# Optimization experiments

Measured on AMD Instinct MI355X. Metric: run time of the kernel, lower is better.

The kernel has to match this reference:

```python
import jax, jax.numpy as jnp
import numpy as np

D_MODEL = 512
NUM_HEADS = 8
DEPTH = D_MODEL // NUM_HEADS
B, S = 8, 1024


def setup_inputs() -> dict:
    key = jax.random.key(0)
    ks = jax.random.split(key, 14)
    scale = 1.0 / np.sqrt(D_MODEL)
    inp = {
        "q_in": jax.random.normal(ks[0], (B, S, D_MODEL), jnp.float32),
        "k_in": jax.random.normal(ks[1], (B, S, D_MODEL), jnp.float32),
        "v_in": jax.random.normal(ks[2], (B, S, D_MODEL), jnp.float32),
        # padding mask: 1 = masked-out position
        "mask": jax.random.randint(ks[3], (B, 1, 1, S), 0, 2).astype(jnp.float32),
        "additional_weights": jax.random.uniform(ks[4], (B, S, S), jnp.float32),
        "wq": jax.random.normal(ks[5], (D_MODEL, D_MODEL), jnp.float32) * scale,
        "bq": jnp.zeros((D_MODEL,), jnp.float32),
        "wk": jax.random.normal(ks[6], (D_MODEL, D_MODEL), jnp.float32) * scale,
        "bk": jnp.zeros((D_MODEL,), jnp.float32),
        "wv": jax.random.normal(ks[7], (D_MODEL, D_MODEL), jnp.float32) * scale,
        "bv": jnp.zeros((D_MODEL,), jnp.float32),
        "wo": jax.random.normal(ks[8], (D_MODEL, D_MODEL), jnp.float32) * scale,
        "bo": jnp.zeros((D_MODEL,), jnp.float32),
    }
    return inp


def _split_heads(x):
    # [B, S, d_model] -> [B, H, S, depth]
    b, s, _ = x.shape
    return x.reshape(b, s, NUM_HEADS, DEPTH).transpose(0, 2, 1, 3)


def reference(q_in, k_in, v_in, mask, additional_weights,
              wq, bq, wk, bk, wv, bv, wo, bo):
    q = _split_heads(q_in @ wq + bq)  # [B,H,S,D]
    k = _split_heads(k_in @ wk + bk)
    v = _split_heads(v_in @ wv + bv)

    scores = jnp.einsum("bhqd,bhkd->bhqk", q, k) / jnp.sqrt(
        jnp.asarray(DEPTH, q.dtype))
    scores = scores + mask * -1e9
    attn = jax.nn.softmax(scores, axis=-1)
    # post-softmax multiplicative weights, broadcast over heads
    attn = attn * additional_weights[:, None, :, :]
    x = jnp.einsum("bhqk,bhkd->bhqd", attn, v)
    x = x.transpose(0, 2, 1, 3).reshape(q_in.shape[0], -1, D_MODEL)
    out = x @ wo + bo
    return out, attn
```

## Files before the change

kernel.cpp:

```cpp
#include <hip/hip_runtime.h>
#include <stdint.h>

typedef unsigned short u16;
typedef short bf16x8 __attribute__((ext_vector_type(8)));
typedef short bf16x4 __attribute__((ext_vector_type(4)));
typedef float f32x4 __attribute__((ext_vector_type(4)));
typedef u16 u16x8 __attribute__((ext_vector_type(8)));
typedef u16 u16x4 __attribute__((ext_vector_type(4)));

#define NHEADS 8
#define SEQ 1024
#define DM 512
#define DEPTH 64
#define BATCH 8
#define BK 32
#define LDSROW 40

__device__ __forceinline__ u16 f2bf(float f) {
    union { float f; unsigned u; } v; v.f = f;
    unsigned r = v.u + 0x7FFF + ((v.u >> 16) & 1);
    return (u16)(r >> 16);
}

__device__ __forceinline__ f32x4 mfma_16x16x16_bf16(bf16x4 a, bf16x4 b, f32x4 c) {
#if __has_builtin(__builtin_amdgcn_mfma_f32_16x16x16bf16_1k)
    return __builtin_amdgcn_mfma_f32_16x16x16bf16_1k(a, b, c, 0, 0, 0);
#else
    asm("v_mfma_f32_16x16x16_bf16 %0, %1, %2, %0" : "+v"(c) : "v"(a), "v"(b));
    return c;
#endif
}

__global__ void __launch_bounds__(256) transpose512(
    const float* __restrict__ w0, const float* __restrict__ w1,
    const float* __restrict__ w2, const float* __restrict__ w3,
    u16* __restrict__ wt)
{
    __shared__ float tile[32][33];
    const float* w = (blockIdx.z == 0) ? w0 : (blockIdx.z == 1) ? w1
                   : (blockIdx.z == 2) ? w2 : w3;
    u16* o = wt + (size_t)blockIdx.z * (DM * DM);
    int rb = blockIdx.y * 32, cb = blockIdx.x * 32;
    int tx = threadIdx.x, ty = threadIdx.y;
    #pragma unroll
    for (int k = 0; k < 32; k += 8)
        tile[ty + k][tx] = w[(size_t)(rb + ty + k) * DM + cb + tx];
    __syncthreads();
    #pragma unroll
    for (int k = 0; k < 32; k += 8)
        o[(size_t)(cb + ty + k) * DM + rb + tx] = f2bf(tile[tx][ty + k]);
}

template <int LAYOUT, int AF32>
__device__ __forceinline__ void gemm_tile2(
    const void* __restrict__ Asrc, const u16* __restrict__ wt,
    const float* __restrict__ bias, void* __restrict__ out_)
{
    __shared__ u16 Al[2][128 * LDSROW];
    __shared__ u16 Bl[2][128 * LDSROW];

    const int tid = threadIdx.x;
    const int wid = tid >> 6, lane = tid & 63;
    const int wm = wid >> 1, wn = wid & 1;
    const int lr = lane & 15, g = lane >> 4, lk = g * 8;
    const int mb = blockIdx.y * 128;
    const int nb = blockIdx.x * 128;
    const int r0 = tid >> 2;
    const int c0 = (tid & 3) * 8;

    f32x4 fa0a, fa0b, fa1a, fa1b;
    u16x8 ua0, ua1, ub0, ub1;

    auto loadStage = [&](int ks) {
        if (AF32) {
            const float* A = (const float*)Asrc;
            fa0a = *(const f32x4*)(A + (size_t)(mb + r0) * DM + ks + c0);
            fa0b = *(const f32x4*)(A + (size_t)(mb + r0) * DM + ks + c0 + 4);
            fa1a = *(const f32x4*)(A + (size_t)(mb + 64 + r0) * DM + ks + c0);
            fa1b = *(const f32x4*)(A + (size_t)(mb + 64 + r0) * DM + ks + c0 + 4);
        } else {
            const u16* A = (const u16*)Asrc;
            ua0 = *(const u16x8*)(A + (size_t)(mb + r0) * DM + ks + c0);
            ua1 = *(const u16x8*)(A + (size_t)(mb + 64 + r0) * DM + ks + c0);
        }
        ub0 = *(const u16x8*)(wt + (size_t)(nb + r0) * DM + ks + c0);
        ub1 = *(const u16x8*)(wt + (size_t)(nb + 64 + r0) * DM + ks + c0);
    };
    auto writeStage = [&](int buf) {
        u16x8 w0, w1;
        if (AF32) {
            #pragma unroll
            for (int j = 0; j < 4; j++) {
                w0[j] = f2bf(fa0a[j]); w0[j + 4] = f2bf(fa0b[j]);
                w1[j] = f2bf(fa1a[j]); w1[j + 4] = f2bf(fa1b[j]);
            }
        } else { w0 = ua0; w1 = ua1; }
        *(u16x8*)(&Al[buf][r0 * LDSROW + c0]) = w0;
        *(u16x8*)(&Al[buf][(64 + r0) * LDSROW + c0]) = w1;
        *(u16x8*)(&Bl[buf][r0 * LDSROW + c0]) = ub0;
        *(u16x8*)(&Bl[buf][(64 + r0) * LDSROW + c0]) = ub1;
    };

    f32x4 acc[4][4];
    #pragma unroll
    for (int i = 0; i < 4; i++)
        #pragma unroll
        for (int j = 0; j < 4; j++) acc[i][j] = (f32x4)0.f;

    loadStage(0);
    for (int ks = 0, step = 0; ks < DM; ks += BK, step++) {
        const int buf = step & 1;
        writeStage(buf);
        if (ks + BK < DM) loadStage(ks + BK);
        __syncthreads();

        bf16x8 af[4], bf4[4];
        #pragma unroll
        for (int mt = 0; mt < 4; mt++)
            af[mt] = *(const bf16x8*)(&Al[buf][(wm * 64 + mt * 16 + lr) * LDSROW + lk]);
        #pragma unroll
        for (int nt = 0; nt < 4; nt++)
            bf4[nt] = *(const bf16x8*)(&Bl[buf][(wn * 64 + nt * 16 + lr) * LDSROW + lk]);
        #pragma unroll
        for (int mt = 0; mt < 4; mt++)
            #pragma unroll
            for (int nt = 0; nt < 4; nt++) {
                if (LAYOUT == 1)
                    acc[mt][nt] = __builtin_amdgcn_mfma_f32_16x16x32_bf16(
                        bf4[nt], af[mt], acc[mt][nt], 0, 0, 0);
                else
                    acc[mt][nt] = __builtin_amdgcn_mfma_f32_16x16x32_bf16(
                        af[mt], bf4[nt], acc[mt][nt], 0, 0, 0);
            }
    }

    #pragma unroll
    for (int mt = 0; mt < 4; mt++) {
        #pragma unroll
        for (int nt = 0; nt < 4; nt++) {
            #pragma unroll
            for (int r = 0; r < 4; r++) {
                if (LAYOUT == 1) {
                    int m = mb + wm * 64 + mt * 16 + lr;
                    int n = nb + wn * 64 + nt * 16 + 4 * g + r;
                    float val = acc[mt][nt][r] + bias[n];
                    int b_ = m >> 10, s = m & 1023, h = n >> 6, d = n & 63;
                    ((u16*)out_)[((size_t)((b_ * NHEADS + h) << 6) + d) * SEQ + s] = f2bf(val);
                } else {
                    int n = nb + wn * 64 + nt * 16 + lr;
                    int m = mb + wm * 64 + mt * 16 + 4 * g + r;
                    float val = acc[mt][nt][r] + bias[n];
                    if (LAYOUT == 2) {
                        ((float*)out_)[(size_t)m * DM + n] = val;
                    } else {
                        int b_ = m >> 10, s = m & 1023, h = n >> 6, d = n & 63;
                        ((u16*)out_)[(((size_t)(b_ * NHEADS + h) * SEQ + s) << 6) + d] = f2bf(val);
                    }
                }
            }
        }
    }
}

__global__ void __launch_bounds__(256) qkv_proj(
    const float* __restrict__ q_in, const float* __restrict__ k_in,
    const float* __restrict__ v_in, const u16* __restrict__ wt_base,
    const float* __restrict__ bq, const float* __restrict__ bk,
    const float* __restrict__ bv,
    u16* __restrict__ Qb, u16* __restrict__ Kb, u16* __restrict__ VTb)
{
    int z = blockIdx.z;
    if (z == 0)      gemm_tile2<0, 1>(q_in, wt_base,              bq, Qb);
    else if (z == 1) gemm_tile2<0, 1>(k_in, wt_base + DM * DM,    bk, Kb);
    else             gemm_tile2<1, 1>(v_in, wt_base + 2 * DM * DM, bv, VTb);
}

__global__ void __launch_bounds__(256) out_proj(
    const u16* __restrict__ X, const u16* __restrict__ wto,
    const float* __restrict__ bo, float* __restrict__ out)
{
    gemm_tile2<2, 0>(X, wto, bo, out);
}

__global__ void __launch_bounds__(256, 5) attn_kernel(
    const u16* __restrict__ Q, const u16* __restrict__ K,
    const u16* __restrict__ VT, const float* __restrict__ mask,
    const float* __restrict__ addw, float* __restrict__ attn_out,
    u16* __restrict__ X)
{
    __shared__ float Xr[4][16][64];
    __shared__ float redm[4][16];
    __shared__ float reds[4][16];

    const int id = blockIdx.x;
    const int c = id & 7, t = id >> 3;
    const int h = t & 7;
    const int p = ((t >> 3) << 3) | c;
    const int qt = p & 63, b = p >> 6;

    const int tid = threadIdx.x, wid = tid >> 6, lane = tid & 63;
    const int lr = lane & 15, g = lane >> 4, lk = g * 8;
    const size_t head = (size_t)(b * NHEADS + h) * (SEQ * DEPTH);
    const u16* Qh = Q + head + (size_t)qt * 16 * DEPTH;
    const u16* Kh = K + head;
    const u16* Vh = VT + head;
    const int wbase = wid << 8;

    bf16x8 qf0 = *(const bf16x8*)(Qh + lr * DEPTH + lk);
    bf16x8 qf1 = *(const bf16x8*)(Qh + lr * DEPTH + 32 + lk);
    f32x4 acc[16];
    #pragma unroll
    for (int nt = 0; nt < 16; nt++) acc[nt] = (f32x4)0.f;
    #pragma unroll
    for (int nt = 0; nt < 16; nt++) {
        const u16* kp = Kh + (size_t)(wbase + (nt << 4) + lr) * DEPTH + lk;
        bf16x8 k0 = *(const bf16x8*)kp;
        bf16x8 k1 = *(const bf16x8*)(kp + 32);
        acc[nt] = __builtin_amdgcn_mfma_f32_16x16x32_bf16(k0, qf0, acc[nt], 0, 0, 0);
        acc[nt] = __builtin_amdgcn_mfma_f32_16x16x32_bf16(k1, qf1, acc[nt], 0, 0, 0);
    }

    const float* mrow = mask + ((size_t)b << 10);
    float mx = -3.0e38f;
    #pragma unroll
    for (int nt = 0; nt < 16; nt++) {
        f32x4 mr = *(const f32x4*)(mrow + wbase + (nt << 4) + 4 * g);
        #pragma unroll
        for (int r = 0; r < 4; r++) {
            acc[nt][r] = acc[nt][r] * 0.125f + mr[r] * -1e9f;
            mx = fmaxf(mx, acc[nt][r]);
        }
    }
    mx = fmaxf(mx, __shfl_xor(mx, 16, 64));
    mx = fmaxf(mx, __shfl_xor(mx, 32, 64));
    if (lane < 16) redm[wid][lr] = mx;
    __syncthreads();
    float gm = fmaxf(fmaxf(redm[0][lr], redm[1][lr]),
                     fmaxf(redm[2][lr], redm[3][lr]));

    float sm = 0.f;
    #pragma unroll
    for (int nt = 0; nt < 16; nt++)
        #pragma unroll
        for (int r = 0; r < 4; r++) {
            float pv = __expf(acc[nt][r] - gm);
            acc[nt][r] = pv;
            sm += pv;
        }
    sm += __shfl_xor(sm, 16, 64);
    sm += __shfl_xor(sm, 32, 64);
    if (lane < 16) reds[wid][lr] = sm;
    __syncthreads();
    float iv = 1.0f / (reds[0][lr] + reds[1][lr] + reds[2][lr] + reds[3][lr]);

    const int qglob = (qt << 4) + lr;
    const size_t awbase = ((size_t)((b << 10) + qglob)) << 10;
    const size_t aobase = ((size_t)(((b * NHEADS + h) << 10) + qglob)) << 10;
    const u16* vb_base = Vh + (size_t)lr * SEQ;

    f32x4 x[4];
    #pragma unroll
    for (int dt = 0; dt < 4; dt++) x[dt] = (f32x4)0.f;

    #pragma unroll
    for (int nt = 0; nt < 16; nt++) {
        const int kk = wbase + (nt << 4) + 4 * g;
        f32x4 aw = *(const f32x4*)(addw + awbase + kk);
        f32x4 o;
        bf16x4 pa;
        #pragma unroll
        for (int r = 0; r < 4; r++) {
            float v = acc[nt][r] * iv * aw[r];
            o[r] = v;
            pa[r] = (short)f2bf(v);
        }
        *(f32x4*)(attn_out + aobase + kk) = o;
        #pragma unroll
        for (int dt = 0; dt < 4; dt++) {
            bf16x4 vb = *(const bf16x4*)(vb_base + (size_t)(dt << 4) * SEQ + kk);
            x[dt] = mfma_16x16x16_bf16(pa, vb, x[dt]);
        }
    }

    #pragma unroll
    for (int dt = 0; dt < 4; dt++)
        #pragma unroll
        for (int r = 0; r < 4; r++)
            Xr[wid][4 * g + r][(dt << 4) + lr] = x[dt][r];
    __syncthreads();

    #pragma unroll
    for (int r = 0; r < 4; r++) {
        int q = 4 * g + r, d = (wid << 4) + lr;
        float s = Xr[0][q][d] + Xr[1][q][d] + Xr[2][q][d] + Xr[3][q][d];
        X[((size_t)((b << 10) + (qt << 4) + q)) * DM + (h << 6) + d] = f2bf(s);
    }
}

extern "C" void kernel_launch(void* const* d_in, const int* in_sizes, int n_in,
                              void* d_out, int out_size, void* d_ws, size_t ws_size,
                              hipStream_t stream)
{
    const float* q_in = (const float*)d_in[0];
    const float* k_in = (const float*)d_in[1];
    const float* v_in = (const float*)d_in[2];
    const float* mask = (const float*)d_in[3];
    const float* addw = (const float*)d_in[4];
    const float* wq = (const float*)d_in[5];
    const float* bq = (const float*)d_in[6];
    const float* wk = (const float*)d_in[7];
    const float* bk = (const float*)d_in[8];
    const float* wv = (const float*)d_in[9];
    const float* bv = (const float*)d_in[10];
    const float* wo = (const float*)d_in[11];
    const float* bo = (const float*)d_in[12];

    const size_t ACT = (size_t)BATCH * SEQ * DM;

    u16* ws = (u16*)d_ws;
    u16* wt  = ws;
    u16* Qb  = wt + 4 * DM * DM;
    u16* Kb  = Qb + ACT;
    u16* VTb = Kb + ACT;
    u16* Xb  = VTb + ACT;

    float* out0 = (float*)d_out;
    float* attn_out = out0 + ACT;

    transpose512<<<dim3(16, 16, 4), dim3(32, 8), 0, stream>>>(wq, wk, wv, wo, wt);
    qkv_proj<<<dim3(4, 64, 3), 256, 0, stream>>>(q_in, k_in, v_in, wt,
                                                 bq, bk, bv, Qb, Kb, VTb);
    attn_kernel<<<dim3(4096), 256, 0, stream>>>(Qb, Kb, VTb, mask, addw,
                                                attn_out, Xb);
    out_proj<<<dim3(4, 64, 1), 256, 0, stream>>>(Xb, wt + 3 * DM * DM, bo, out0);
}
```

Measured before the change: 602.1 us.

## Restructure attention block to 512 threads with LDS-staged P for PV MFMA

The attention kernel now uses 8 waves per 16-query tile, so each wave covers 128 keys. Probabilities are written as bf16 into a padded LDS buffer. The PV product is then redone with 16x16x32 MFMAs, each wave taking one 16-wide depth slice over half the keys, with a 2-way cross-wave reduction. The grid changes to a 3D (head, qtile, batch) order, which drops the old block-id swizzle that grouped heads for addw reuse. Nontemporal loads and stores are added for the streaming addw/attn outputs and the GEMM epilogues. The aim is more parallelism and wider MFMAs, at the cost of extra LDS traffic and a third barrier.

```diff
diff --git a/kernel.cpp b/kernel.cpp
--- a/kernel.cpp
+++ b/kernel.cpp
@@ -15,6 +15,7 @@
 #define BATCH 8
 #define BK 32
 #define LDSROW 40
+#define PSTRIDE 1032
 
 __device__ __forceinline__ u16 f2bf(float f) {
     union { float f; unsigned u; } v; v.f = f;
@@ -22,12 +23,20 @@
     return (u16)(r >> 16);
 }
 
-__device__ __forceinline__ f32x4 mfma_16x16x16_bf16(bf16x4 a, bf16x4 b, f32x4 c) {
-#if __has_builtin(__builtin_amdgcn_mfma_f32_16x16x16bf16_1k)
-    return __builtin_amdgcn_mfma_f32_16x16x16bf16_1k(a, b, c, 0, 0, 0);
+template <typename T>
+__device__ __forceinline__ void st_nt(T* p, T v) {
+#if __has_builtin(__builtin_nontemporal_store)
+    __builtin_nontemporal_store(v, p);
 #else
-    asm("v_mfma_f32_16x16x16_bf16 %0, %1, %2, %0" : "+v"(c) : "v"(a), "v"(b));
-    return c;
+    *p = v;
+#endif
+}
+template <typename T>
+__device__ __forceinline__ T ld_nt(const T* p) {
+#if __has_builtin(__builtin_nontemporal_load)
+    return __builtin_nontemporal_load(p);
+#else
+    return *p;
 #endif
 }
 
@@ -145,16 +154,16 @@
                     int n = nb + wn * 64 + nt * 16 + 4 * g + r;
                     float val = acc[mt][nt][r] + bias[n];
                     int b_ = m >> 10, s = m & 1023, h = n >> 6, d = n & 63;
-                    ((u16*)out_)[((size_t)((b_ * NHEADS + h) << 6) + d) * SEQ + s] = f2bf(val);
+                    st_nt(&((u16*)out_)[((size_t)((b_ * NHEADS + h) << 6) + d) * SEQ + s], f2bf(val));
                 } else {
                     int n = nb + wn * 64 + nt * 16 + lr;
                     int m = mb + wm * 64 + mt * 16 + 4 * g + r;
                     float val = acc[mt][nt][r] + bias[n];
                     if (LAYOUT == 2) {
-                        ((float*)out_)[(size_t)m * DM + n] = val;
+                        st_nt(&((float*)out_)[(size_t)m * DM + n], val);
                     } else {
                         int b_ = m >> 10, s = m & 1023, h = n >> 6, d = n & 63;
-                        ((u16*)out_)[(((size_t)(b_ * NHEADS + h) * SEQ + s) << 6) + d] = f2bf(val);
+                        st_nt(&((u16*)out_)[(((size_t)(b_ * NHEADS + h) * SEQ + s) << 6) + d], f2bf(val));
                     }
                 }
             }
@@ -170,8 +179,8 @@
     u16* __restrict__ Qb, u16* __restrict__ Kb, u16* __restrict__ VTb)
 {
     int z = blockIdx.z;
-    if (z == 0)      gemm_tile2<0, 1>(q_in, wt_base,              bq, Qb);
-    else if (z == 1) gemm_tile2<0, 1>(k_in, wt_base + DM * DM,    bk, Kb);
+    if (z == 0)      gemm_tile2<0, 1>(q_in, wt_base,               bq, Qb);
+    else if (z == 1) gemm_tile2<0, 1>(k_in, wt_base + DM * DM,     bk, Kb);
     else             gemm_tile2<1, 1>(v_in, wt_base + 2 * DM * DM, bv, VTb);
 }
 
@@ -182,37 +191,33 @@
     gemm_tile2<2, 0>(X, wto, bo, out);
 }
 
-__global__ void __launch_bounds__(256, 5) attn_kernel(
+__global__ void __launch_bounds__(512, 6) attn_kernel(
     const u16* __restrict__ Q, const u16* __restrict__ K,
     const u16* __restrict__ VT, const float* __restrict__ mask,
     const float* __restrict__ addw, float* __restrict__ attn_out,
     u16* __restrict__ X)
 {
-    __shared__ float Xr[4][16][64];
-    __shared__ float redm[4][16];
-    __shared__ float reds[4][16];
-
-    const int id = blockIdx.x;
-    const int c = id & 7, t = id >> 3;
-    const int h = t & 7;
-    const int p = ((t >> 3) << 3) | c;
-    const int qt = p & 63, b = p >> 6;
-
+    __shared__ u16 Pl[16 * PSTRIDE];
+    __shared__ float Xr[2][16][64];
+    __shared__ float redm[8][16];
+    __shared__ float reds[8][16];
+
+    const int h = blockIdx.x, qt = blockIdx.y, b = blockIdx.z;
     const int tid = threadIdx.x, wid = tid >> 6, lane = tid & 63;
     const int lr = lane & 15, g = lane >> 4, lk = g * 8;
     const size_t head = (size_t)(b * NHEADS + h) * (SEQ * DEPTH);
     const u16* Qh = Q + head + (size_t)qt * 16 * DEPTH;
     const u16* Kh = K + head;
     const u16* Vh = VT + head;
-    const int wbase = wid << 8;
+    const int wbase = wid << 7;
 
     bf16x8 qf0 = *(const bf16x8*)(Qh + lr * DEPTH + lk);
     bf16x8 qf1 = *(const bf16x8*)(Qh + lr * DEPTH + 32 + lk);
-    f32x4 acc[16];
-    #pragma unroll
-    for (int nt = 0; nt < 16; nt++) acc[nt] = (f32x4)0.f;
-    #pragma unroll
-    for (int nt = 0; nt < 16; nt++) {
+    f32x4 acc[8];
+    #pragma unroll
+    for (int nt = 0; nt < 8; nt++) acc[nt] = (f32x4)0.f;
+    #pragma unroll
+    for (int nt = 0; nt < 8; nt++) {
         const u16* kp = Kh + (size_t)(wbase + (nt << 4) + lr) * DEPTH + lk;
         bf16x8 k0 = *(const bf16x8*)kp;
         bf16x8 k1 = *(const bf16x8*)(kp + 32);
@@ -223,7 +228,7 @@
     const float* mrow = mask + ((size_t)b << 10);
     float mx = -3.0e38f;
     #pragma unroll
-    for (int nt = 0; nt < 16; nt++) {
+    for (int nt = 0; nt < 8; nt++) {
         f32x4 mr = *(const f32x4*)(mrow + wbase + (nt << 4) + 4 * g);
         #pragma unroll
         for (int r = 0; r < 4; r++) {
@@ -235,12 +240,13 @@
     mx = fmaxf(mx, __shfl_xor(mx, 32, 64));
     if (lane < 16) redm[wid][lr] = mx;
     __syncthreads();
-    float gm = fmaxf(fmaxf(redm[0][lr], redm[1][lr]),
-                     fmaxf(redm[2][lr], redm[3][lr]));
+    float gm = redm[0][lr];
+    #pragma unroll
+    for (int w = 1; w < 8; w++) gm = fmaxf(gm, redm[w][lr]);
 
     float sm = 0.f;
     #pragma unroll
-    for (int nt = 0; nt < 16; nt++)
+    for (int nt = 0; nt < 8; nt++)
         #pragma unroll
         for (int r = 0; r < 4; r++) {
             float pv = __expf(acc[nt][r] - gm);
@@ -251,49 +257,51 @@
     sm += __shfl_xor(sm, 32, 64);
     if (lane < 16) reds[wid][lr] = sm;
     __syncthreads();
-    float iv = 1.0f / (reds[0][lr] + reds[1][lr] + reds[2][lr] + reds[3][lr]);
+    float sv = reds[0][lr];
+    #pragma unroll
+    for (int w = 1; w < 8; w++) sv += reds[w][lr];
+    float iv = 1.0f / sv;
 
     const int qglob = (qt << 4) + lr;
     const size_t awbase = ((size_t)((b << 10) + qglob)) << 10;
     const size_t aobase = ((size_t)(((b * NHEADS + h) << 10) + qglob)) << 10;
-    const u16* vb_base = Vh + (size_t)lr * SEQ;
-
-    f32x4 x[4];
-    #pragma unroll
-    for (int dt = 0; dt < 4; dt++) x[dt] = (f32x4)0.f;
-
-    #pragma unroll
-    for (int nt = 0; nt < 16; nt++) {
+    #pragma unroll
+    for (int nt = 0; nt < 8; nt++) {
         const int kk = wbase + (nt << 4) + 4 * g;
-        f32x4 aw = *(const f32x4*)(addw + awbase + kk);
+        f32x4 aw = ld_nt((const f32x4*)(addw + awbase + kk));
         f32x4 o;
-        bf16x4 pa;
+        u16x4 pb;
         #pragma unroll
         for (int r = 0; r < 4; r++) {
             float v = acc[nt][r] * iv * aw[r];
             o[r] = v;
-            pa[r] = (short)f2bf(v);
-        }
-        *(f32x4*)(attn_out + aobase + kk) = o;
-        #pragma unroll
-        for (int dt = 0; dt < 4; dt++) {
-            bf16x4 vb = *(const bf16x4*)(vb_base + (size_t)(dt << 4) * SEQ + kk);
-            x[dt] = mfma_16x16x16_bf16(pa, vb, x[dt]);
-        }
-    }
-
-    #pragma unroll
-    for (int dt = 0; dt < 4; dt++)
-        #pragma unroll
-        for (int r = 0; r < 4; r++)
-            Xr[wid][4 * g + r][(dt << 4) + lr] = x[dt][r];
-    __syncthreads();
-
-    #pragma unroll
-    for (int r = 0; r < 4; r++) {
-        int q = 4 * g + r, d = (wid << 4) + lr;
-        float s = Xr[0][q][d] + Xr[1][q][d] + Xr[2][q][d] + Xr[3][q][d];
-        X[((size_t)((b << 10) + (qt << 4) + q)) * DM + (h << 6) + d] = f2bf(s);
+            pb[r] = f2bf(v);
+        }
+        st_nt((f32x4*)(attn_out + aobase + kk), o);
+        *(u16x4*)(Pl + lr * PSTRIDE + kk) = pb;
+    }
+    __syncthreads();
+
+    const int kh = wid >> 2, dq = wid & 3;
+    f32x4 x = (f32x4)0.f;
+    const u16* vrow = Vh + (size_t)((dq << 4) + lr) * SEQ;
+    const int ks0 = kh << 9;
+    for (int ks = ks0; ks < ks0 + 512; ks += 32) {
+        bf16x8 a = *(const bf16x8*)(Pl + lr * PSTRIDE + ks + lk);
+        bf16x8 bv = *(const bf16x8*)(vrow + ks + lk);
+        x = __builtin_amdgcn_mfma_f32_16x16x32_bf16(a, bv, x, 0, 0, 0);
+    }
+    #pragma unroll
+    for (int r = 0; r < 4; r++)
+        Xr[kh][4 * g + r][(dq << 4) + lr] = x[r];
+    __syncthreads();
+
+    #pragma unroll
+    for (int rr = 0; rr < 2; rr++) {
+        int q = 4 * g + (kh << 1) + rr;
+        int d = (dq << 4) + lr;
+        float s = Xr[0][q][d] + Xr[1][q][d];
+        st_nt(&X[((size_t)((b << 10) + (qt << 4) + q)) * DM + (h << 6) + d], f2bf(s));
     }
 }
 
@@ -330,7 +338,7 @@
     transpose512<<<dim3(16, 16, 4), dim3(32, 8), 0, stream>>>(wq, wk, wv, wo, wt);
     qkv_proj<<<dim3(4, 64, 3), 256, 0, stream>>>(q_in, k_in, v_in, wt,
                                                  bq, bk, bv, Qb, Kb, VTb);
-    attn_kernel<<<dim3(4096), 256, 0, stream>>>(Qb, Kb, VTb, mask, addw,
-                                                attn_out, Xb);
+    attn_kernel<<<dim3(8, 64, 8), 512, 0, stream>>>(Qb, Kb, VTb, mask, addw,
+                                                    attn_out, Xb);
     out_proj<<<dim3(4, 64, 1), 256, 0, stream>>>(Xb, wt + 3 * DM * DM, bo, out0);
 }
```

Result: slower. 631.6 us (+4.9%).
